# Performance work log

Measured on AMD Instinct MI355X. Metric: run time of the kernel, lower is better.

The kernel has to match this reference:

```python
import jax, jax.numpy as jnp
import numpy as np

# ---- hardcoded module constants (from Cyborg.__init__) ----
B, S, V = 256, 128, 512
H = 30              # number of symbol vectors
N_STACKS = 2
R = 2               # REDUNDANCY
DEPTH = 4           # stack_depth
ZERO_OFFSET = 1e-6
NAND_BIAS = 3.0
INIT_SHARPEN = 10.0
N_VECS = 1 + N_STACKS  # input vec + one peek per stack = 3
C_BIG = (H + N_STACKS) * R   # 64 choices for push_fn / calc_out
C_SMALL = 2 * R              # 4 choices for pop_op / push_op


def _cossim(a, b, eps=1e-8):
    # torch.cosine_similarity semantics: per-vector norm clamp
    na = jnp.maximum(jnp.linalg.norm(a, axis=-1, keepdims=True), eps)
    nb = jnp.maximum(jnp.linalg.norm(b, axis=-1, keepdims=True), eps)
    return jnp.sum((a / na) * (b / nb), axis=-1)


def _nand(query, w, nw_raw):
    # Fuzzy-NAND gate bank (neurallambda NAND, clip='abs').
    # query: [B, N_VECS*V], w: [C, N_VECS*V], nw_raw: [C, N_VECS] -> [B, C]
    C = w.shape[0]
    q = query.reshape(-1, 1, N_VECS, V)
    wv = w.reshape(1, C, N_VECS, V)
    cos = jnp.abs(_cossim(q, wv))                 # [B, C, N_VECS], clip='abs'
    nw = jax.nn.sigmoid(nw_raw)[None]             # interpolate sim vs NOT(sim)
    interp = nw * cos + (1.0 - nw) * (1.0 - cos)
    return jnp.prod(interp, axis=-1)              # fuzzy AND over the 3 vecs


# ---- differentiable stack (soft pointer over DEPTH slots) ----
def _read(stack, ptr):
    return jnp.einsum('bdv,bd->bv', stack, ptr)

def _push(stack, ptr, val):
    p = jnp.roll(ptr, 1, axis=1)
    s = stack * (1.0 - p)[..., None] + val[:, None, :] * p[..., None]
    return s, p

def _pop(stack, ptr):
    s = stack * (1.0 - ptr)[..., None] + ZERO_OFFSET * ptr[..., None]
    p = jnp.roll(ptr, -1, axis=1)
    return s, p

def _pop_or_nop(stack, ptr, sharp, should_pop, should_nop):
    pr = jax.nn.softmax(jnp.stack([should_pop, should_nop], -1) * sharp, axis=-1)
    ps, pp = _pop(stack, ptr)
    s = ps * pr[:, 0, None, None] + stack * pr[:, 1, None, None]
    p = pp * pr[:, 0, None] + ptr * pr[:, 1, None]
    return s, p

def _push_or_nop(stack, ptr, sharp, should_push, should_nop, val):
    pr = jax.nn.softmax(jnp.stack([should_push, should_nop], -1) * sharp, axis=-1)
    ps, pp = _push(stack, ptr, val)
    s = ps * pr[:, 0, None, None] + stack * pr[:, 1, None, None]
    p = pp * pr[:, 0, None] + ptr * pr[:, 1, None]
    return s, p


def _forward(x, syms, stack_init_vec, sharp, pop_w, pop_nw, pushop_w, pushop_nw,
             pushfn_w, pushfn_nw, calc_w, calc_nw):
    b = x.shape[0]
    # init both stacks to zero_offset, pointer at slot 0, then hard-push init vec
    stack0 = jnp.full((N_STACKS, b, DEPTH, V), ZERO_OFFSET, x.dtype)
    ptr0 = jnp.zeros((N_STACKS, b, DEPTH), x.dtype).at[:, :, 0].set(1.0)
    init_val = jnp.broadcast_to(stack_init_vec, (b, V))
    stack0, ptr0 = jax.vmap(_push, in_axes=(0, 0, None))(stack0, ptr0, init_val)

    syms_b = jnp.broadcast_to(syms, (b, H, V))

    def step(carry, inp):
        stacks, ptrs = carry                                    # [2,B,D,V], [2,B,D]
        peeks = jax.vmap(_read)(stacks, ptrs)                   # [2,B,V]
        inps = jnp.concatenate([inp, peeks[0], peeks[1]], -1)   # [B,3V]
        out_opts = jnp.concatenate(
            [syms_b, peeks[0][:, None], peeks[1][:, None]], 1)  # [B,H+2,V]
        new_s, new_p = [], []
        for k in range(N_STACKS):
            pops = _nand(inps, pop_w[k], pop_nw[k])             # [B, 2R]
            pushes = _nand(inps, pushop_w[k], pushop_nw[k])     # [B, 2R]
            pv = _nand(inps, pushfn_w[k], pushfn_nw[k]).reshape(b, H + N_STACKS, R)
            push_val = jnp.einsum('bcv,bcr->bv', out_opts, pv)
            s, p = _pop_or_nop(stacks[k], ptrs[k], sharp[k],
                               pops[:, :R].max(1), pops[:, R:].max(1))
            s, p = _push_or_nop(s, p, sharp[k],
                                pushes[:, :R].max(1), pushes[:, R:].max(1), push_val)
            new_s.append(s)
            new_p.append(p)
        stacks = jnp.stack(new_s)
        ptrs = jnp.stack(new_p)
        peeks2 = jax.vmap(_read)(stacks, ptrs)
        inps2 = jnp.concatenate([inp, peeks2[0], peeks2[1]], -1)
        out_opts2 = jnp.concatenate(
            [syms_b, peeks2[0][:, None], peeks2[1][:, None]], 1)
        cv = _nand(inps2, calc_w, calc_nw).reshape(b, H + N_STACKS, R)
        out = jnp.einsum('bcv,bcr->bv', out_opts2, cv)
        return (stacks, ptrs), out

    _, outs = jax.lax.scan(step, (stack0, ptr0), jnp.swapaxes(x, 0, 1))
    return jnp.swapaxes(outs, 0, 1)  # [B,S,V]


def setup_inputs() -> dict:
    key = jax.random.key(0)
    ks = jax.random.split(key, 12)
    siv = jax.random.normal(ks[1], (V,), jnp.float32)
    siv = siv / jnp.linalg.norm(siv)
    return {
        'x': jax.random.normal(ks[0], (B, S, V), jnp.float32),
        'syms': jax.random.normal(ks[2], (H, V), jnp.float32),
        'stack_init_vec': siv,
        'sharp': jnp.full((N_STACKS,), INIT_SHARPEN, jnp.float32),
        'pop_w': jax.random.normal(ks[3], (N_STACKS, C_SMALL, N_VECS * V), jnp.float32),
        'pop_nw': jax.random.normal(ks[4], (N_STACKS, C_SMALL, N_VECS), jnp.float32) + NAND_BIAS,
        'pushop_w': jax.random.normal(ks[5], (N_STACKS, C_SMALL, N_VECS * V), jnp.float32),
        'pushop_nw': jax.random.normal(ks[6], (N_STACKS, C_SMALL, N_VECS), jnp.float32) + NAND_BIAS,
        'pushfn_w': jax.random.normal(ks[7], (N_STACKS, C_BIG, N_VECS * V), jnp.float32),
        'pushfn_nw': jax.random.normal(ks[8], (N_STACKS, C_BIG, N_VECS), jnp.float32) + NAND_BIAS,
        'calc_w': jax.random.normal(ks[9], (C_BIG, N_VECS * V), jnp.float32),
        'calc_nw': jax.random.normal(ks[10], (C_BIG, N_VECS), jnp.float32) + NAND_BIAS,
    }


def reference(x, syms, stack_init_vec, sharp, pop_w, pop_nw, pushop_w, pushop_nw,
              pushfn_w, pushfn_nw, calc_w, calc_nw):
    return _forward(x, syms, stack_init_vec, sharp, pop_w, pop_nw, pushop_w,
                    pushop_nw, pushfn_w, pushfn_nw, calc_w, calc_nw)
```

## Files before the change

### kernel.cpp

```cpp
#include <hip/hip_runtime.h>
#include <math.h>


#define SS 128
#define VV 512
#define NROWS 208
#define ZOFF 1e-6f

#define OFF_I0   0
#define OFF_OC   (32768*208)
#define OFF_GI   (OFF_OC + 32768*32)
#define OFF_M    (OFF_GI + 2*32*208)
#define OFF_A    (OFF_M + 1024)
#define OFF_Bc   (OFF_A + 624)
#define OFF_W0   (OFF_Bc + 624)

typedef _Float16 half8 __attribute__((ext_vector_type(8)));
typedef float f32x4 __attribute__((ext_vector_type(4)));
typedef float f32x2 __attribute__((ext_vector_type(2)));

__device__ __forceinline__ float rlane(float v, int lane) {
    return __int_as_float(__builtin_amdgcn_readlane(__float_as_int(v), lane));
}
template <int CTRL>
__device__ __forceinline__ float dpp_add(float x) {
    int y = __builtin_amdgcn_update_dpp(0, __float_as_int(x), CTRL, 0xF, 0xF, true);
    return x + __int_as_float(y);
}
__device__ __forceinline__ float sum16(float x) {
    x = dpp_add<0xB1>(x);
    x = dpp_add<0x4E>(x);
    x = dpp_add<0x124>(x);
    x = dpp_add<0x128>(x);
    return x;
}
__device__ __forceinline__ float swz16(float x) {
    return __int_as_float(__builtin_amdgcn_ds_swizzle(__float_as_int(x), 0x401F));
}

__device__ __forceinline__ const float* w_row(int r, const float* pw, const float* pow_,
                                              const float* pfw, const float* cw) {
    if (r < 8)   return pw   + r * 1536;
    if (r < 16)  return pow_ + (r - 8) * 1536;
    if (r < 144) return pfw  + (r - 16) * 1536;
    return cw + (r - 144) * 1536;
}
__device__ __forceinline__ const float* nw_row(int r, const float* pn, const float* pon,
                                               const float* pfn, const float* cn) {
    if (r < 8)   return pn   + r * 3;
    if (r < 16)  return pon  + (r - 8) * 3;
    if (r < 144) return pfn  + (r - 16) * 3;
    return cn + (r - 144) * 3;
}

__global__ void kB(const float* __restrict__ syms, const float* __restrict__ siv,
                   const float* __restrict__ pw, const float* __restrict__ pn,
                   const float* __restrict__ pow_, const float* __restrict__ pon,
                   const float* __restrict__ pfw, const float* __restrict__ pfn,
                   const float* __restrict__ cw, const float* __restrict__ cn,
                   float* __restrict__ ws) {
    int blk = blockIdx.x, tid = threadIdx.x;
    if (blk < 64) {
        int jj = blk >> 5, e = blk & 31;
        __shared__ float bas[512];
        for (int i = tid; i < 512; i += 256)
            bas[i] = (e == 0) ? 1.0f : ((e == 1) ? siv[i] : syms[(e - 2) * 512 + i]);
        __syncthreads();
        if (tid < NROWS) {
            int c = tid;
            const float4* w4 = (const float4*)(w_row(c, pw, pow_, pfw, cw) + (jj + 1) * 512);
            const float4* b4 = (const float4*)bas;
            float s = 0.f;
            for (int q = 0; q < 128; ++q) {
                float4 a = b4[q], b = w4[q];
                s += a.x * b.x + a.y * b.y + a.z * b.z + a.w * b.w;
            }
            ws[OFF_GI + (jj * 32 + e) * 208 + c] = s;
        }
    } else if (blk == 64) {
        __shared__ float basw[32 * 512];
        for (int i = tid; i < 32 * 512; i += 256) {
            int m = i >> 9, v = i & 511;
            basw[i] = (m == 0) ? 1.0f : ((m == 1) ? siv[v] : syms[(m - 2) * 512 + v]);
        }
        __syncthreads();
        for (int p = tid; p < 1024; p += 256) {
            int m = p >> 5, mm = p & 31;
            const float4* a4 = (const float4*)(basw + m * 512);
            const float4* b4 = (const float4*)(basw + mm * 512);
            float s = 0.f;
            for (int q = 0; q < 128; ++q) {
                float4 a = a4[q], b = b4[q];
                s += a.x * b.x + a.y * b.y + a.z * b.z + a.w * b.w;
            }
            ws[OFF_M + p] = s;
        }
    } else if (blk == 65) {
        for (int idx = tid; idx < 624; idx += 256) {
            int r = idx / 3, j = idx % 3;
            const float4* w4 = (const float4*)(w_row(r, pw, pow_, pfw, cw) + j * 512);
            float s = 0.f;
            for (int q = 0; q < 128; ++q) {
                float4 b = w4[q];
                s += b.x * b.x + b.y * b.y + b.z * b.z + b.w * b.w;
            }
            float nrm = fmaxf(sqrtf(s), 1e-8f);
            float nwv = nw_row(r, pn, pon, pfn, cn)[j];
            float sig = 1.f / (1.f + expf(-nwv));
            ws[OFF_A + idx]  = (2.f * sig - 1.f) / nrm;
            ws[OFF_Bc + idx] = 1.f - sig;
        }
    } else {
        int part = blk - 66;
        _Float16* whp = (_Float16*)(ws + OFF_W0);
        _Float16* wlp = whp + 208 * 512;
        for (int i = tid; i < 6656; i += 256) {
            int flat = part * 6656 + i;
            int c = flat >> 9, v = flat & 511;
            float wv = w_row(c, pw, pow_, pfw, cw)[v];
            _Float16 h = (_Float16)wv;
            whp[flat] = h;
            wlp[flat] = (_Float16)(wv - (float)h);
        }
    }
}

__global__ __launch_bounds__(256) void kA(const float* __restrict__ x, float* __restrict__ ws) {
    __shared__ half8 AH[2][256];
    __shared__ half8 AL[2][256];
    __shared__ float red[256];
    __shared__ float invx[64];
    const int tid = threadIdx.x;
    const int wid = tid >> 6, l = tid & 63;
    const int bid = blockIdx.x;
    const size_t bt0 = (size_t)(bid >> 1) * 64;

    const int sr = tid >> 2, ss = tid & 3;
    const float* xp = x + (bt0 + sr) * 512 + ss * 8;
    const int wpos = (sr >> 4) * 64 + (sr & 15) + (ss << 4);

    const _Float16* whp = (const _Float16*)(ws + OFF_W0);
    const _Float16* wlp = whp + 208 * 512;

    const int gw = ((bid & 1) << 2) | wid;
    const int nt = (gw < 5) ? 2 : 1;
    const int t0 = (gw < 5) ? (2 * gw) : (5 + gw);

    f32x4 acc[4][2];
#pragma unroll
    for (int m = 0; m < 4; ++m)
#pragma unroll
        for (int tt = 0; tt < 2; ++tt)
            acc[m][tt] = (f32x4){0.f, 0.f, 0.f, 0.f};

    float sumsq = 0.f;

    {
        float v[8];
        *(float4*)v       = *(const float4*)(xp);
        *(float4*)(v + 4) = *(const float4*)(xp + 4);
        half8 hh, hl;
#pragma unroll
        for (int j = 0; j < 8; ++j) {
            sumsq += v[j] * v[j];
            _Float16 h = (_Float16)v[j];
            hh[j] = h;
            hl[j] = (_Float16)(v[j] - (float)h);
        }
        AH[0][wpos] = hh;
        AL[0][wpos] = hl;
    }
    __syncthreads();

    for (int kt = 0; kt < 16; ++kt) {
        const int buf = kt & 1;
        half8 ahm[4], alm[4];
#pragma unroll
        for (int m = 0; m < 4; ++m) {
            ahm[m] = AH[buf][m * 64 + l];
            alm[m] = AL[buf][m * 64 + l];
        }
        float4 xv0, xv1;
        if (kt < 15) {
            xv0 = *(const float4*)(xp + (kt + 1) * 32);
            xv1 = *(const float4*)(xp + (kt + 1) * 32 + 4);
        }
        const int kof = kt * 32 + (l >> 4) * 8;
#pragma unroll
        for (int tt = 0; tt < 2; ++tt) {
            if (tt < nt) {
                const int c = (t0 + tt) * 16 + (l & 15);
                half8 bh = *(const half8*)(whp + c * 512 + kof);
                half8 bl = *(const half8*)(wlp + c * 512 + kof);
#pragma unroll
                for (int m = 0; m < 4; ++m) {
                    acc[m][tt] = __builtin_amdgcn_mfma_f32_16x16x32_f16(ahm[m], bh, acc[m][tt], 0, 0, 0);
                    acc[m][tt] = __builtin_amdgcn_mfma_f32_16x16x32_f16(ahm[m], bl, acc[m][tt], 0, 0, 0);
                    acc[m][tt] = __builtin_amdgcn_mfma_f32_16x16x32_f16(alm[m], bh, acc[m][tt], 0, 0, 0);
                }
            }
        }
        if (kt < 15) {
            float v[8];
            *(float4*)v = xv0; *(float4*)(v + 4) = xv1;
            half8 hh, hl;
#pragma unroll
            for (int j = 0; j < 8; ++j) {
                sumsq += v[j] * v[j];
                _Float16 h = (_Float16)v[j];
                hh[j] = h;
                hl[j] = (_Float16)(v[j] - (float)h);
            }
            AH[buf ^ 1][wpos] = hh;
            AL[buf ^ 1][wpos] = hl;
        }
        __syncthreads();
    }

    red[tid] = sumsq;
    __syncthreads();
    if (tid < 64) {
        float s = red[tid * 4] + red[tid * 4 + 1] + red[tid * 4 + 2] + red[tid * 4 + 3];
        invx[tid] = 1.f / fmaxf(sqrtf(s), 1e-8f);
    }
    __syncthreads();

#pragma unroll
    for (int tt = 0; tt < 2; ++tt) {
        if (tt < nt) {
            const int c = (t0 + tt) * 16 + (l & 15);
            const float A0 = ws[OFF_A + c * 3];
            const float B0 = ws[OFF_Bc + c * 3];
#pragma unroll
            for (int m = 0; m < 4; ++m) {
                const int rbase = m * 16 + (l >> 4) * 4;
#pragma unroll
                for (int j = 0; j < 4; ++j) {
                    const float ix = invx[rbase + j];
                    ws[OFF_I0 + (bt0 + rbase + j) * 208 + c] = A0 * fabsf(acc[m][tt][j]) * ix + B0;
                }
            }
        }
    }
}

__global__ __attribute__((amdgpu_flat_work_group_size(256, 256), amdgpu_waves_per_eu(1, 1)))
void kC(float* __restrict__ ws, const float* __restrict__ sharp) {
    __shared__ float nndL[2][144];
    const int b = blockIdx.x, tid = threadIdx.x;
    const int wid = tid >> 6, l = tid & 63;
    const int k = l >> 5, m = l & 31;
    const int isW3 = (wid == 3);
    const int isRow = (tid < 144);
    const int r = isW3 ? (144 + l) : tid;

    const float* GI = ws + OFF_GI;
    f32x2 GM1[32], GM2[32];
#pragma unroll
    for (int i = 0; i < 32; ++i) {
        float mv = ws[OFF_M + m * 32 + i];
        GM1[i] = (f32x2){GI[i * 208 + r], mv};
        GM2[i] = (f32x2){GI[(32 + i) * 208 + r], mv};
    }
    const float A1 = ws[OFF_A + r * 3 + 1],  A2 = ws[OFF_A + r * 3 + 2];
    const float B1 = ws[OFF_Bc + r * 3 + 1], B2 = ws[OFF_Bc + r * 3 + 2];
    const float sh = sharp[k];

    float st[4], p[4];
#pragma unroll
    for (int d = 0; d < 4; ++d) {
        st[d] = (d == 1) ? ((m == 1) ? 1.f : 0.f) : ((m == 0) ? ZOFF : 0.f);
        p[d] = (d == 1) ? 1.f : 0.f;
    }
    float pk = st[0] * p[0] + st[1] * p[1] + st[2] * p[2] + st[3] * p[3];
    float pkOther = __shfl_xor(pk, 32);

    const float* i0base = ws + OFF_I0 + (size_t)b * SS * 208;
    const int ioff = isW3 ? 0 : 1;
    float i0pro = i0base[r];
    float i0use = i0base[(size_t)ioff * 208 + r];

    auto CA = [&](float pp, float po, float iv) -> float {
        f32x2 a1 = (f32x2){0.f, 0.f}, b1 = (f32x2){0.f, 0.f};
        f32x2 a2 = (f32x2){0.f, 0.f}, b2 = (f32x2){0.f, 0.f};
#pragma unroll
        for (int mm = 0; mm < 32; ++mm) {
            float v0 = rlane(pp, mm);
            float v1 = rlane(pp, 32 + mm);
            if (mm & 1) { b1 += GM1[mm] * v0;  b2 += GM2[mm] * v1; }
            else        { a1 += GM1[mm] * v0;  a2 += GM2[mm] * v1; }
        }
        float dd1 = a1.x + b1.x, gq0 = a1.y + b1.y;
        float dd2 = a2.x + b2.x, gq1 = a2.y + b2.y;
        float pm0 = (k ? po : pp) * gq0;
        float pm1 = (k ? pp : po) * gq1;
        float q0 = sum16(pm0); q0 += swz16(q0);
        float q1 = sum16(pm1); q1 += swz16(q1);
        float iq0 = __frsqrt_rn(fmaxf(q0, 1e-16f));
        float iq1 = __frsqrt_rn(fmaxf(q1, 1e-16f));
        return iv * (A1 * fabsf(dd1) * iq0 + B1) * (A2 * fabsf(dd2) * iq1 + B2);
    };

    {
        float nv0 = CA(pk, pkOther, i0pro);
        if (isRow) nndL[0][tid] = nv0;
    }
    __syncthreads();

    for (int t = 0; t < SS; ++t) {
        int nidx = t + 1 + ioff; if (nidx > SS - 1) nidx = SS - 1;
        float i0nxt = i0base[(size_t)nidx * 208 + r];

        const float* nb = nndL[t & 1];
        float4 gp4 = *(const float4*)(nb + 4 * k);
        float4 gq4 = *(const float4*)(nb + 8 + 4 * k);
        float prp0 = 1.f / (1.f + __expf((fmaxf(gp4.z, gp4.w) - fmaxf(gp4.x, gp4.y)) * sh));
        float prq0 = 1.f / (1.f + __expf((fmaxf(gq4.z, gq4.w) - fmaxf(gq4.x, gq4.y)) * sh));
        float prp1 = 1.f - prp0, prq1 = 1.f - prq0;
        float prx = 0.f, pry = 0.f;
        if (m >= 2) {
            float2 pr2 = *(const float2*)(nb + 16 + 64 * k + 2 * m - 4);
            prx = pr2.x; pry = pr2.y;
        }
        float4 t30 = *(const float4*)(nb + 16 + 64 * k + 60);
        float pk0m = k ? pkOther : pk;
        float pk1m = k ? pk : pkOther;
        float pvc = prx + pry + (t30.x + t30.y) * pk0m + (t30.z + t30.w) * pk1m;

        float zc = (m == 0) ? ZOFF : 0.f;
        float s1v[4], p1[4];
#pragma unroll
        for (int d = 0; d < 4; ++d) {
            float ps = st[d] * (1.f - p[d]) + zc * p[d];
            s1v[d] = ps * prp0 + st[d] * prp1;
            p1[d] = p[(d + 1) & 3] * prp0 + p[d] * prp1;
        }
#pragma unroll
        for (int d = 0; d < 4; ++d) {
            float pu = p1[(d + 3) & 3];
            float su = s1v[d] * (1.f - pu) + pvc * pu;
            st[d] = su * prq0 + s1v[d] * prq1;
            p[d] = pu * prq0 + p1[d] * prq1;
        }
        float pkp = st[0] * p[0] + st[1] * p[1] + st[2] * p[2] + st[3] * p[3];
        float pkpOth = __shfl_xor(pkp, 32);

        float nv = CA(pkp, pkpOth, i0use);
        if (isRow) nndL[(t + 1) & 1][tid] = nv;
        if (isW3) {
            float s60 = rlane(nv, 60), s61 = rlane(nv, 61);
            float s62 = rlane(nv, 62), s63 = rlane(nv, 63);
            int src = (m >= 2) ? (2 * m - 4) : 0;
            float cx = __shfl(nv, src);
            float cy = __shfl(nv, src + 1);
            if (m < 2) { cx = 0.f; cy = 0.f; }
            if (l < 32) {
                float oc = cx + cy + (s60 + s61) * pkp + (s62 + s63) * pkpOth;
                ws[OFF_OC + ((size_t)b * SS + t) * 32 + m] = oc;
            }
        }
        __syncthreads();
        pk = pkp;
        pkOther = pkpOth;
        i0use = i0nxt;
    }
}

__global__ __launch_bounds__(256) void kD(const float* __restrict__ ws, const float* __restrict__ syms,
                                          const float* __restrict__ siv, float* __restrict__ out) {
    int t = threadIdx.x;
    int rg = t >> 6;
    int vc = (t & 63) * 8;
    size_t r0 = (size_t)blockIdx.x * 16 + rg * 4;
    const float* oc = ws + OFF_OC;
    float acc[4][8];
    float4 sv0 = *(const float4*)(siv + vc);
    float4 sv1 = *(const float4*)(siv + vc + 4);
#pragma unroll
    for (int rr = 0; rr < 4; ++rr) {
        float c0 = oc[(r0 + rr) * 32 + 0];
        float c1 = oc[(r0 + rr) * 32 + 1];
        acc[rr][0] = c0 + c1 * sv0.x; acc[rr][1] = c0 + c1 * sv0.y;
        acc[rr][2] = c0 + c1 * sv0.z; acc[rr][3] = c0 + c1 * sv0.w;
        acc[rr][4] = c0 + c1 * sv1.x; acc[rr][5] = c0 + c1 * sv1.y;
        acc[rr][6] = c0 + c1 * sv1.z; acc[rr][7] = c0 + c1 * sv1.w;
    }
    for (int mm = 0; mm < 30; ++mm) {
        float4 b0 = *(const float4*)(syms + mm * 512 + vc);
        float4 b1 = *(const float4*)(syms + mm * 512 + vc + 4);
#pragma unroll
        for (int rr = 0; rr < 4; ++rr) {
            float c = oc[(r0 + rr) * 32 + 2 + mm];
            acc[rr][0] += c * b0.x; acc[rr][1] += c * b0.y;
            acc[rr][2] += c * b0.z; acc[rr][3] += c * b0.w;
            acc[rr][4] += c * b1.x; acc[rr][5] += c * b1.y;
            acc[rr][6] += c * b1.z; acc[rr][7] += c * b1.w;
        }
    }
#pragma unroll
    for (int rr = 0; rr < 4; ++rr) {
        float* o = out + (r0 + rr) * 512 + vc;
        *(float4*)o       = make_float4(acc[rr][0], acc[rr][1], acc[rr][2], acc[rr][3]);
        *(float4*)(o + 4) = make_float4(acc[rr][4], acc[rr][5], acc[rr][6], acc[rr][7]);
    }
}

extern "C" void kernel_launch(void* const* d_in, const int* in_sizes, int n_in,
                              void* d_out, int out_size, void* d_ws, size_t ws_size,
                              hipStream_t stream) {
    const float* x    = (const float*)d_in[0];
    const float* syms = (const float*)d_in[1];
    const float* siv  = (const float*)d_in[2];
    const float* shp  = (const float*)d_in[3];
    const float* pw   = (const float*)d_in[4];
    const float* pn   = (const float*)d_in[5];
    const float* pow_ = (const float*)d_in[6];
    const float* pon  = (const float*)d_in[7];
    const float* pfw  = (const float*)d_in[8];
    const float* pfn  = (const float*)d_in[9];
    const float* cw   = (const float*)d_in[10];
    const float* cn   = (const float*)d_in[11];
    float* ws  = (float*)d_ws;
    float* out = (float*)d_out;

    hipLaunchKernelGGL(kB, dim3(82),   dim3(256), 0, stream,
                       syms, siv, pw, pn, pow_, pon, pfw, pfn, cw, cn, ws);
    hipLaunchKernelGGL(kA, dim3(1024), dim3(256), 0, stream, x, ws);
    hipLaunchKernelGGL(kC, dim3(256),  dim3(256), 0, stream, ws, shp);
    hipLaunchKernelGGL(kD, dim3(2048), dim3(256), 0, stream, ws, syms, siv, out);
}
```

Before: 375.8 us.

## Fuse output expansion into recurrent kernel, overlapping with next timestep

Drops the separate output-expansion kernel kD. The recurrent kernel kC now keeps each timestep's 32 output coefficients in double-buffered shared memory and expands them against syms and stack_init_vec one step later, interleaved with the next step's compute. This removes the global round-trip of the coefficient buffer and a kernel launch, and hides the expansion work behind the latency-bound serial loop. In exchange, each thread holds 60 extra registers of syms in a kernel already limited to one wave per EU, and every step issues a global store on the critical loop.

```diff
diff --git a/kernel.cpp b/kernel.cpp
--- a/kernel.cpp
+++ b/kernel.cpp
@@ -245,8 +245,11 @@
 }
 
 __global__ __attribute__((amdgpu_flat_work_group_size(256, 256), amdgpu_waves_per_eu(1, 1)))
-void kC(float* __restrict__ ws, const float* __restrict__ sharp) {
+void kC(float* __restrict__ ws, const float* __restrict__ sharp,
+        const float* __restrict__ syms, const float* __restrict__ siv,
+        float* __restrict__ out) {
     __shared__ float nndL[2][144];
+    __shared__ float ocL[2][32];
     const int b = blockIdx.x, tid = threadIdx.x;
     const int wid = tid >> 6, l = tid & 63;
     const int k = l >> 5, m = l & 31;
@@ -265,6 +268,13 @@
     const float A1 = ws[OFF_A + r * 3 + 1],  A2 = ws[OFF_A + r * 3 + 2];
     const float B1 = ws[OFF_Bc + r * 3 + 1], B2 = ws[OFF_Bc + r * 3 + 2];
     const float sh = sharp[k];
+
+    float2 sv2 = *(const float2*)(siv + 2 * tid);
+    float2 sy[30];
+#pragma unroll
+    for (int mm = 0; mm < 30; ++mm)
+        sy[mm] = *(const float2*)(syms + mm * 512 + 2 * tid);
+    float* outb = out + (size_t)b * SS * 512 + 2 * tid;
 
     float st[4], p[4];
 #pragma unroll
@@ -300,6 +310,22 @@
         float iq1 = __frsqrt_rn(fmaxf(q1, 1e-16f));
         return iv * (A1 * fabsf(dd1) * iq0 + B1) * (A2 * fabsf(dd2) * iq1 + B2);
     };
+    auto expand = [&](int buf, int t) {
+        const float* ocp = ocL[buf];
+        float4 c[8];
+#pragma unroll
+        for (int q = 0; q < 8; ++q) c[q] = *(const float4*)(ocp + 4 * q);
+        float o0 = c[0].x + c[0].y * sv2.x;
+        float o1 = c[0].x + c[0].y * sv2.y;
+#pragma unroll
+        for (int mm = 0; mm < 30; ++mm) {
+            float cv = (mm + 2 < 4) ? ((mm + 2 == 2) ? c[0].z : c[0].w)
+                                    : ((&c[0].x)[mm + 2]);
+            o0 += cv * sy[mm].x;
+            o1 += cv * sy[mm].y;
+        }
+        *(float2*)(outb + (size_t)t * 512) = (float2){o0, o1};
+    };
 
     {
         float nv0 = CA(pk, pkOther, i0pro);
@@ -344,6 +370,8 @@
         }
         float pkp = st[0] * p[0] + st[1] * p[1] + st[2] * p[2] + st[3] * p[3];
         float pkpOth = __shfl_xor(pkp, 32);
+
+        if (t > 0) expand((t - 1) & 1, t - 1);
 
         float nv = CA(pkp, pkpOth, i0use);
         if (isRow) nndL[(t + 1) & 1][tid] = nv;
@@ -356,7 +384,7 @@
             if (m < 2) { cx = 0.f; cy = 0.f; }
             if (l < 32) {
                 float oc = cx + cy + (s60 + s61) * pkp + (s62 + s63) * pkpOth;
-                ws[OFF_OC + ((size_t)b * SS + t) * 32 + m] = oc;
+                ocL[t & 1][m] = oc;
             }
         }
         __syncthreads();
@@ -364,45 +392,7 @@
         pkOther = pkpOth;
         i0use = i0nxt;
     }
-}
-
-__global__ __launch_bounds__(256) void kD(const float* __restrict__ ws, const float* __restrict__ syms,
-                                          const float* __restrict__ siv, float* __restrict__ out) {
-    int t = threadIdx.x;
-    int rg = t >> 6;
-    int vc = (t & 63) * 8;
-    size_t r0 = (size_t)blockIdx.x * 16 + rg * 4;
-    const float* oc = ws + OFF_OC;
-    float acc[4][8];
-    float4 sv0 = *(const float4*)(siv + vc);
-    float4 sv1 = *(const float4*)(siv + vc + 4);
-#pragma unroll
-    for (int rr = 0; rr < 4; ++rr) {
-        float c0 = oc[(r0 + rr) * 32 + 0];
-        float c1 = oc[(r0 + rr) * 32 + 1];
-        acc[rr][0] = c0 + c1 * sv0.x; acc[rr][1] = c0 + c1 * sv0.y;
-        acc[rr][2] = c0 + c1 * sv0.z; acc[rr][3] = c0 + c1 * sv0.w;
-        acc[rr][4] = c0 + c1 * sv1.x; acc[rr][5] = c0 + c1 * sv1.y;
-        acc[rr][6] = c0 + c1 * sv1.z; acc[rr][7] = c0 + c1 * sv1.w;
-    }
-    for (int mm = 0; mm < 30; ++mm) {
-        float4 b0 = *(const float4*)(syms + mm * 512 + vc);
-        float4 b1 = *(const float4*)(syms + mm * 512 + vc + 4);
-#pragma unroll
-        for (int rr = 0; rr < 4; ++rr) {
-            float c = oc[(r0 + rr) * 32 + 2 + mm];
-            acc[rr][0] += c * b0.x; acc[rr][1] += c * b0.y;
-            acc[rr][2] += c * b0.z; acc[rr][3] += c * b0.w;
-            acc[rr][4] += c * b1.x; acc[rr][5] += c * b1.y;
-            acc[rr][6] += c * b1.z; acc[rr][7] += c * b1.w;
-        }
-    }
-#pragma unroll
-    for (int rr = 0; rr < 4; ++rr) {
-        float* o = out + (r0 + rr) * 512 + vc;
-        *(float4*)o       = make_float4(acc[rr][0], acc[rr][1], acc[rr][2], acc[rr][3]);
-        *(float4*)(o + 4) = make_float4(acc[rr][4], acc[rr][5], acc[rr][6], acc[rr][7]);
-    }
+    expand((SS - 1) & 1, SS - 1);
 }
 
 extern "C" void kernel_launch(void* const* d_in, const int* in_sizes, int n_in,
@@ -426,6 +416,5 @@
     hipLaunchKernelGGL(kB, dim3(82),   dim3(256), 0, stream,
                        syms, siv, pw, pn, pow_, pon, pfw, pfn, cw, cn, ws);
     hipLaunchKernelGGL(kA, dim3(1024), dim3(256), 0, stream, x, ws);
-    hipLaunchKernelGGL(kC, dim3(256),  dim3(256), 0, stream, ws, shp);
-    hipLaunchKernelGGL(kD, dim3(2048), dim3(256), 0, stream, ws, syms, siv, out);
-}
+    hipLaunchKernelGGL(kC, dim3(256),  dim3(256), 0, stream, ws, shp, syms, siv, out);
+}
```

New measurement: 358.6 us. -4.6%, faster.
